# Kernel optimization log

Hardware: AMD Instinct MI355X
Metric: run time of the kernel (lower is better)

The kernel has to match this reference:

```python
import jax, jax.numpy as jnp
import numpy as np

D_MODEL = 1024
MAX_LEN = 2048
BATCH = 4


def _causal_mask(max_len):
    # tril ones -> 0 on/below diag, -inf above (added to scores BEFORE scaling,
    # matching the original module's order of operations)
    return jnp.where(jnp.tril(jnp.ones((max_len, max_len), dtype=bool)), 0.0, -jnp.inf).astype(jnp.float32)


def setup_inputs() -> dict:
    key = jax.random.key(0)
    ks = jax.random.split(key, 9)
    s = 1.0 / np.sqrt(D_MODEL)  # torch Linear default init scale (uniform bound)
    return {
        "encoded_q": jax.random.normal(ks[0], (BATCH, MAX_LEN, D_MODEL), jnp.float32),
        "encoded_k": jax.random.normal(ks[1], (BATCH, MAX_LEN, D_MODEL), jnp.float32),
        "encoded_v": jax.random.normal(ks[2], (BATCH, MAX_LEN, D_MODEL), jnp.float32),
        "W_q": jax.random.uniform(ks[3], (D_MODEL, D_MODEL), jnp.float32, -s, s),
        "b_q": jax.random.uniform(ks[4], (D_MODEL,), jnp.float32, -s, s),
        "W_k": jax.random.uniform(ks[5], (D_MODEL, D_MODEL), jnp.float32, -s, s),
        "b_k": jax.random.uniform(ks[6], (D_MODEL,), jnp.float32, -s, s),
        "W_v": jax.random.uniform(ks[7], (D_MODEL, D_MODEL), jnp.float32, -s, s),
        "b_v": jax.random.uniform(ks[8], (D_MODEL,), jnp.float32, -s, s),
        "parameter_mask": 1,
    }


def reference(encoded_q, encoded_k, encoded_v, W_q, b_q, W_k, b_k, W_v, b_v, parameter_mask):
    # torch Linear: y = x @ W.T + b
    q = jnp.einsum("bsd,ed->bse", encoded_q, W_q) + b_q  # [B,S,D]
    k = jnp.einsum("bsd,ed->bse", encoded_k, W_k) + b_k
    v = jnp.einsum("bsd,ed->bse", encoded_v, W_v) + b_v
    values = jnp.einsum("bqd,bkd->bqk", q, k)  # [B,S,S]
    if parameter_mask:
        values = values + _causal_mask(values.shape[-1])
    scaled = values / jnp.sqrt(jnp.float32(D_MODEL))
    attn = jax.nn.softmax(scaled, axis=-1)
    return jnp.einsum("bqk,bkd->bqd", attn, v)  # [B,S,D]
```

## Files before the change

kernel.cpp:

```cpp
#include <hip/hip_runtime.h>

typedef __bf16 bf16;
typedef __attribute__((ext_vector_type(8))) __bf16 bf16x8;
typedef __attribute__((ext_vector_type(4))) __bf16 bf16x4;
typedef __attribute__((ext_vector_type(4))) float f32x4;

#define S_LEN 2048
#define DM 1024
#define NB 4

__device__ __forceinline__ void async_copy16(const void* g, void* l)
{
    __builtin_amdgcn_global_load_lds(
        (const __attribute__((address_space(1))) unsigned int*)g,
        (__attribute__((address_space(3))) unsigned int*)l,
        16, 0, 0);
}

__device__ __forceinline__ void gemm_tile(
    const bf16* __restrict__ A, int lda,
    const bf16* __restrict__ B, int ldb,
    int kSteps, char* smem, f32x4 (&acc)[4][4])
{
    bf16* sA = (bf16*)smem;
    bf16* sB = (bf16*)(smem + 16384);
    const int tid = threadIdx.x;
    const int w = tid >> 6, lane = tid & 63;
    const int quad = lane >> 4, l16 = lane & 15;
    const int wr = w >> 1, wc = w & 1;

#pragma unroll
    for (int i = 0; i < 4; i++)
#pragma unroll
        for (int j = 0; j < 4; j++) acc[i][j] = f32x4{0.f, 0.f, 0.f, 0.f};

    const int srow = tid >> 3;
    const int sc8  = tid & 7;
    const int srcCol = (sc8 ^ (srow & 7)) * 16;
    const char* aG = (const char*)(A + (size_t)srow * lda) + srcCol;
    const char* bG = (const char*)(B + (size_t)srow * ldb) + srcCol;
    char* aL = (char*)sA + w * 1024;
    char* bL = (char*)sB + w * 1024;
    const size_t aRow32 = (size_t)lda * 64;
    const size_t bRow32 = (size_t)ldb * 64;

    const int swz = l16 & 7;

    for (int ks = 0; ks < kSteps; ks++) {
        const char* aGk = aG + (size_t)ks * 128;
        const char* bGk = bG + (size_t)ks * 128;
#pragma unroll
        for (int i = 0; i < 4; i++) {
            async_copy16(aGk + i * aRow32, aL + i * 4096);
            async_copy16(bGk + i * bRow32, bL + i * 4096);
        }
        __syncthreads();
#pragma unroll
        for (int kk = 0; kk < 2; kk++) {
            bf16x8 af[4], bfr[4];
#pragma unroll
            for (int t = 0; t < 4; t++) {
                const int ca = ((kk * 4 + quad) ^ swz) * 16;
                af[t]  = *(const bf16x8*)((const char*)sA + (wr * 64 + t * 16 + l16) * 128 + ca);
                bfr[t] = *(const bf16x8*)((const char*)sB + (wc * 64 + t * 16 + l16) * 128 + ca);
            }
#pragma unroll
            for (int rt = 0; rt < 4; rt++)
#pragma unroll
                for (int ct = 0; ct < 4; ct++)
                    acc[rt][ct] = __builtin_amdgcn_mfma_f32_16x16x32_bf16(
                        af[rt], bfr[ct], acc[rt][ct], 0, 0, 0);
        }
        __syncthreads();
    }
}

__global__ __launch_bounds__(256) void cvt3_kernel(
    const float* __restrict__ s0, const float* __restrict__ s1, const float* __restrict__ s2,
    bf16* __restrict__ d0, bf16* __restrict__ d1, bf16* __restrict__ d2)
{
    const float* src = blockIdx.y == 0 ? s0 : blockIdx.y == 1 ? s1 : s2;
    bf16* dst        = blockIdx.y == 0 ? d0 : blockIdx.y == 1 ? d1 : d2;
    size_t i = ((size_t)blockIdx.x * 256 + threadIdx.x) * 8;
    f32x4 a = *(const f32x4*)(src + i);
    f32x4 b = *(const f32x4*)(src + i + 4);
    bf16x8 o;
    o[0] = (bf16)a[0]; o[1] = (bf16)a[1]; o[2] = (bf16)a[2]; o[3] = (bf16)a[3];
    o[4] = (bf16)b[0]; o[5] = (bf16)b[1]; o[6] = (bf16)b[2]; o[7] = (bf16)b[3];
    *(bf16x8*)(dst + i) = o;
}

__global__ __launch_bounds__(256) void proj_kernel(
    const bf16* __restrict__ Eq, const bf16* __restrict__ Ek, const bf16* __restrict__ Ev,
    const bf16* __restrict__ Wq, const bf16* __restrict__ Wk, const bf16* __restrict__ Wv,
    const float* __restrict__ bq, const float* __restrict__ bk, const float* __restrict__ bv,
    bf16* __restrict__ Qo, bf16* __restrict__ Ko, bf16* __restrict__ Vt)
{
    __shared__ __align__(16) char smem[34816];
    const int bid = blockIdx.x;
    const int c = bid & 7;
    const int j = bid >> 3;
    const int z = j >> 6;
    const int r64 = j & 63;
    const int mTile = c * 8 + (r64 >> 3);
    const int nTile = r64 & 7;
    const int m0 = mTile * 128, n0 = nTile * 128;

    const bf16* E     = z == 0 ? Eq : z == 1 ? Ek : Ev;
    const bf16* W     = z == 0 ? Wq : z == 1 ? Wk : Wv;
    const float* bias = z == 0 ? bq : z == 1 ? bk : bv;

    f32x4 acc[4][4];
    gemm_tile(E + (size_t)m0 * DM, DM, W + (size_t)n0 * DM, DM, DM / 64, smem, acc);

    const int tid = threadIdx.x;
    const int w = tid >> 6, lane = tid & 63;
    const int quad = lane >> 4, l16 = lane & 15;
    const int wr = w >> 1, wc = w & 1;
    const int nBase = n0 + wc * 64;

    float bcol[4];
#pragma unroll
    for (int ct = 0; ct < 4; ct++) bcol[ct] = bias[nBase + ct * 16 + l16];

    if (z < 2) {
        bf16* Tt = (bf16*)smem;
#pragma unroll
        for (int rt = 0; rt < 4; rt++)
#pragma unroll
            for (int ct = 0; ct < 4; ct++)
#pragma unroll
                for (int r = 0; r < 4; r++)
                    Tt[(wr * 64 + rt * 16 + quad * 4 + r) * 136 + wc * 64 + ct * 16 + l16]
                        = (bf16)(acc[rt][ct][r] + bcol[ct]);
        __syncthreads();
        bf16* O = z == 0 ? Qo : Ko;
        const int row = tid >> 1, half = tid & 1;
        const bf16* src = Tt + row * 136 + half * 64;
        bf16* dst = O + (size_t)(m0 + row) * DM + n0 + half * 64;
#pragma unroll
        for (int i = 0; i < 8; i++)
            *(bf16x8*)(dst + i * 8) = *(const bf16x8*)(src + i * 8);
    } else {
        const int mBase = m0 + wr * 64;
#pragma unroll
        for (int rt = 0; rt < 4; rt++) {
            const int m = mBase + rt * 16 + quad * 4;
            const int bb = m >> 11;
            const int s  = m & 2047;
#pragma unroll
            for (int ct = 0; ct < 4; ct++) {
                const int n = nBase + ct * 16 + l16;
                bf16x4 o;
                o[0] = (bf16)(acc[rt][ct][0] + bcol[ct]);
                o[1] = (bf16)(acc[rt][ct][1] + bcol[ct]);
                o[2] = (bf16)(acc[rt][ct][2] + bcol[ct]);
                o[3] = (bf16)(acc[rt][ct][3] + bcol[ct]);
                *(bf16x4*)(Vt + ((size_t)(bb * DM + n)) * S_LEN + s) = o;
            }
        }
    }
}

__global__ __launch_bounds__(256) void qk_kernel(
    const bf16* __restrict__ Q, const bf16* __restrict__ K,
    const int* __restrict__ maskp, bf16* __restrict__ P, float* __restrict__ lsum)
{
    const int bid = blockIdx.x;
    const int c = bid & 7;
    const int j = bid >> 3;
    const int b = j >> 5;
    const int jj = j & 31;
    const int kt = (jj < 16) ? c : (15 - c);
    const int qt = jj & 15;
    const bool causal = (maskp[0] != 0);
    if (causal && kt > qt) return;

    __shared__ __align__(16) char smem[34816];

    f32x4 acc[4][4];
    const bf16* Qb = Q + ((size_t)(b * S_LEN + qt * 128)) * DM;
    const bf16* Kb = K + ((size_t)(b * S_LEN + kt * 128)) * DM;
    gemm_tile(Qb, DM, Kb, DM, DM / 64, smem, acc);

    const int tid = threadIdx.x;
    const int w = tid >> 6, lane = tid & 63;
    const int quad = lane >> 4, l16 = lane & 15;
    const int wr = w >> 1, wc = w & 1;
    const float scale = 0.03125f;

    bf16* Pt = (bf16*)smem;
#pragma unroll
    for (int rt = 0; rt < 4; rt++)
#pragma unroll
        for (int r = 0; r < 4; r++) {
            const int rloc = wr * 64 + rt * 16 + quad * 4 + r;
            const int qg = qt * 128 + rloc;
#pragma unroll
            for (int ct = 0; ct < 4; ct++) {
                const int kg = kt * 128 + wc * 64 + ct * 16 + l16;
                float p = (!causal || kg <= qg) ? __expf(acc[rt][ct][r] * scale) : 0.0f;
                Pt[rloc * 136 + wc * 64 + ct * 16 + l16] = (bf16)p;
            }
        }
    __syncthreads();

    bf16* Pb = P + (size_t)b * S_LEN * S_LEN;
    float* lb = lsum + b * S_LEN;
    const int row = tid >> 1, half = tid & 1;
    const bf16* src = Pt + row * 136 + half * 64;
    bf16* dst = Pb + (size_t)(qt * 128 + row) * S_LEN + kt * 128 + half * 64;
    float rs = 0.0f;
#pragma unroll
    for (int i = 0; i < 8; i++) {
        bf16x8 x = *(const bf16x8*)(src + i * 8);
        *(bf16x8*)(dst + i * 8) = x;
#pragma unroll
        for (int e = 0; e < 8; e++) rs += (float)x[e];
    }
    rs += __shfl_xor(rs, 1);
    if (half == 0) atomicAdd(&lb[qt * 128 + row], rs);
}

__global__ __launch_bounds__(256) void pv_kernel(
    const bf16* __restrict__ P, const bf16* __restrict__ Vt,
    const float* __restrict__ lsum, const int* __restrict__ maskp,
    float* __restrict__ Out)
{
    const int bid = blockIdx.x;
    const int dt = bid & 7;
    const int j = bid >> 3;
    const int b = j >> 4;
    const int qt = 15 - (j & 15);
    const bool causal = (maskp[0] != 0);
    const int kSteps = causal ? (qt + 1) * 2 : (S_LEN / 64);

    __shared__ __align__(16) char smem[33792];

    f32x4 acc[4][4];
    const bf16* Pb = P + ((size_t)b * S_LEN + qt * 128) * S_LEN;
    const bf16* Vb = Vt + ((size_t)(b * DM + dt * 128)) * S_LEN;
    gemm_tile(Pb, S_LEN, Vb, S_LEN, kSteps, smem, acc);

    const int tid = threadIdx.x;
    const int w = tid >> 6, lane = tid & 63;
    const int quad = lane >> 4, l16 = lane & 15;
    const int wr = w >> 1, wc = w & 1;

    const float* lb = lsum + b * S_LEN;
    float inv[4][4];
#pragma unroll
    for (int rt = 0; rt < 4; rt++)
#pragma unroll
        for (int r = 0; r < 4; r++)
            inv[rt][r] = 1.0f / lb[qt * 128 + wr * 64 + rt * 16 + quad * 4 + r];

    float* Ot = (float*)smem;
#pragma unroll
    for (int h = 0; h < 2; h++) {
        if (wr == h) {
#pragma unroll
            for (int rt = 0; rt < 4; rt++)
#pragma unroll
                for (int r = 0; r < 4; r++) {
                    const int rloc = rt * 16 + quad * 4 + r;
#pragma unroll
                    for (int ct = 0; ct < 4; ct++)
                        Ot[rloc * 132 + wc * 64 + ct * 16 + l16] = acc[rt][ct][r] * inv[rt][r];
                }
        }
        __syncthreads();
        const int row = tid >> 2, qq = tid & 3;
        const float* src = Ot + row * 132 + qq * 32;
        float* dst = Out + (size_t)(b * S_LEN + qt * 128 + h * 64 + row) * DM + dt * 128 + qq * 32;
#pragma unroll
        for (int i = 0; i < 8; i++)
            *(f32x4*)(dst + i * 4) = *(const f32x4*)(src + i * 4);
        __syncthreads();
    }
}

extern "C" void kernel_launch(void* const* d_in, const int* in_sizes, int n_in,
                              void* d_out, int out_size, void* d_ws, size_t ws_size,
                              hipStream_t stream)
{
    const float* Eq = (const float*)d_in[0];
    const float* Ek = (const float*)d_in[1];
    const float* Ev = (const float*)d_in[2];
    const float* Wq = (const float*)d_in[3];
    const float* bq = (const float*)d_in[4];
    const float* Wk = (const float*)d_in[5];
    const float* bk = (const float*)d_in[6];
    const float* Wv = (const float*)d_in[7];
    const float* bv = (const float*)d_in[8];
    const int* maskp = (const int*)d_in[9];
    float* Out = (float*)d_out;

    char* ws = (char*)d_ws;
    const size_t SZ_QKV = (size_t)NB * S_LEN * DM * 2;
    const size_t SZ_W   = (size_t)DM * DM * 2;
    bf16* Qb  = (bf16*)(ws);
    bf16* Kb  = (bf16*)(ws + SZ_QKV);
    bf16* Vtb = (bf16*)(ws + 2 * SZ_QKV);
    bf16* Wqb = (bf16*)(ws + 3 * SZ_QKV);
    bf16* Wkb = (bf16*)(ws + 3 * SZ_QKV + SZ_W);
    bf16* Wvb = (bf16*)(ws + 3 * SZ_QKV + 2 * SZ_W);
    float* lsum = (float*)(ws + 3 * SZ_QKV + 3 * SZ_W);
    bf16* Pbuf = (bf16*)(ws + 3 * SZ_QKV + 3 * SZ_W + (1 << 20));
    bf16* Eqb = Pbuf;
    bf16* Ekb = Eqb + (size_t)NB * S_LEN * DM;
    bf16* Evb = Ekb + (size_t)NB * S_LEN * DM;

    hipMemsetAsync(lsum, 0, (size_t)NB * S_LEN * 4, stream);
    cvt3_kernel<<<dim3(512, 3), 256, 0, stream>>>(Wq, Wk, Wv, Wqb, Wkb, Wvb);
    cvt3_kernel<<<dim3(4096, 3), 256, 0, stream>>>(Eq, Ek, Ev, Eqb, Ekb, Evb);

    proj_kernel<<<1536, 256, 0, stream>>>(
        Eqb, Ekb, Evb, Wqb, Wkb, Wvb, bq, bk, bv, Qb, Kb, Vtb);

    qk_kernel<<<1024, 256, 0, stream>>>(Qb, Kb, maskp, Pbuf, lsum);
    pv_kernel<<<512, 256, 0, stream>>>(Pbuf, Vtb, lsum, maskp, Out);
}
```

Before: 314.3 us.

## Double-buffer LDS tiles in gemm_tile with async prefetch of next k-step

Rewrites the shared GEMM mainloop so each block keeps two LDS buffers. It issues the global-to-LDS async loads for step k+2 while the MFMAs for the current step run, using explicit vmcnt/lgkmcnt waits and raw barriers. The aim is to hide global load latency that the old load-sync-compute-sync loop exposed. In exchange LDS per block grows to 64 KB, which may lower occupancy, and the loop assumes an even kSteps. Extra syncthreads are added before the epilogues reuse shared memory.

```diff
diff --git a/kernel.cpp b/kernel.cpp
--- a/kernel.cpp
+++ b/kernel.cpp
@@ -17,13 +17,58 @@
         16, 0, 0);
 }
 
+#define VM_WAIT8 asm volatile("s_waitcnt vmcnt(8)" ::: "memory")
+#define VM_WAIT0 asm volatile("s_waitcnt vmcnt(0)" ::: "memory")
+#define LGKM0    asm volatile("s_waitcnt lgkmcnt(0)" ::: "memory")
+#define BAR      asm volatile("s_barrier" ::: "memory")
+
+
+__device__ __forceinline__ void stage_issue(const char* aGk, size_t aRow32,
+                                            const char* bGk, size_t bRow32,
+                                            char* aL, char* bL)
+{
+#pragma unroll
+    for (int i = 0; i < 4; i++) {
+        async_copy16(aGk + i * aRow32, aL + i * 4096);
+        async_copy16(bGk + i * bRow32, bL + i * 4096);
+    }
+}
+
+__device__ __forceinline__ void read_frags(const char* bufA, const char* bufB,
+                                           int wr, int wc, int l16, int quad,
+                                           bf16x8 (&af)[2][4], bf16x8 (&bfr)[2][4])
+{
+    const int swz = l16 & 7;
+#pragma unroll
+    for (int kk = 0; kk < 2; kk++) {
+        const int col = (((kk << 2) + quad) ^ swz) << 4;
+#pragma unroll
+        for (int t = 0; t < 4; t++) {
+            af[kk][t]  = *(const bf16x8*)(bufA + (wr * 64 + t * 16 + l16) * 128 + col);
+            bfr[kk][t] = *(const bf16x8*)(bufB + (wc * 64 + t * 16 + l16) * 128 + col);
+        }
+    }
+}
+
+__device__ __forceinline__ void mfma_all(const bf16x8 (&af)[2][4],
+                                         const bf16x8 (&bfr)[2][4],
+                                         f32x4 (&acc)[4][4])
+{
+#pragma unroll
+    for (int kk = 0; kk < 2; kk++)
+#pragma unroll
+        for (int rt = 0; rt < 4; rt++)
+#pragma unroll
+            for (int ct = 0; ct < 4; ct++)
+                acc[rt][ct] = __builtin_amdgcn_mfma_f32_16x16x32_bf16(
+                    af[kk][rt], bfr[kk][ct], acc[rt][ct], 0, 0, 0);
+}
+
 __device__ __forceinline__ void gemm_tile(
     const bf16* __restrict__ A, int lda,
     const bf16* __restrict__ B, int ldb,
     int kSteps, char* smem, f32x4 (&acc)[4][4])
 {
-    bf16* sA = (bf16*)smem;
-    bf16* sB = (bf16*)(smem + 16384);
     const int tid = threadIdx.x;
     const int w = tid >> 6, lane = tid & 63;
     const int quad = lane >> 4, l16 = lane & 15;
@@ -39,39 +84,39 @@
     const int srcCol = (sc8 ^ (srow & 7)) * 16;
     const char* aG = (const char*)(A + (size_t)srow * lda) + srcCol;
     const char* bG = (const char*)(B + (size_t)srow * ldb) + srcCol;
-    char* aL = (char*)sA + w * 1024;
-    char* bL = (char*)sB + w * 1024;
     const size_t aRow32 = (size_t)lda * 64;
     const size_t bRow32 = (size_t)ldb * 64;
-
-    const int swz = l16 & 7;
-
-    for (int ks = 0; ks < kSteps; ks++) {
-        const char* aGk = aG + (size_t)ks * 128;
-        const char* bGk = bG + (size_t)ks * 128;
-#pragma unroll
-        for (int i = 0; i < 4; i++) {
-            async_copy16(aGk + i * aRow32, aL + i * 4096);
-            async_copy16(bGk + i * bRow32, bL + i * 4096);
-        }
-        __syncthreads();
-#pragma unroll
-        for (int kk = 0; kk < 2; kk++) {
-            bf16x8 af[4], bfr[4];
-#pragma unroll
-            for (int t = 0; t < 4; t++) {
-                const int ca = ((kk * 4 + quad) ^ swz) * 16;
-                af[t]  = *(const bf16x8*)((const char*)sA + (wr * 64 + t * 16 + l16) * 128 + ca);
-                bfr[t] = *(const bf16x8*)((const char*)sB + (wc * 64 + t * 16 + l16) * 128 + ca);
-            }
-#pragma unroll
-            for (int rt = 0; rt < 4; rt++)
-#pragma unroll
-                for (int ct = 0; ct < 4; ct++)
-                    acc[rt][ct] = __builtin_amdgcn_mfma_f32_16x16x32_bf16(
-                        af[rt], bfr[ct], acc[rt][ct], 0, 0, 0);
-        }
-        __syncthreads();
+    char* aL0 = smem +     0 + w * 1024;
+    char* bL0 = smem + 16384 + w * 1024;
+    char* aL1 = smem + 32768 + w * 1024;
+    char* bL1 = smem + 49152 + w * 1024;
+
+    stage_issue(aG,       aRow32, bG,       bRow32, aL0, bL0);
+    stage_issue(aG + 128, aRow32, bG + 128, bRow32, aL1, bL1);
+
+    for (int ks = 0; ks < kSteps; ks += 2) {
+        const bool more = (ks + 2 < kSteps);
+        bf16x8 af[2][4], bfr[2][4];
+
+        VM_WAIT8;
+        BAR;
+        read_frags(smem, smem + 16384, wr, wc, l16, quad, af, bfr);
+        LGKM0;
+        BAR;
+        if (more)
+            stage_issue(aG + (size_t)(ks + 2) * 128, aRow32,
+                        bG + (size_t)(ks + 2) * 128, bRow32, aL0, bL0);
+        mfma_all(af, bfr, acc);
+
+        if (more) { VM_WAIT8; } else { VM_WAIT0; }
+        BAR;
+        read_frags(smem + 32768, smem + 49152, wr, wc, l16, quad, af, bfr);
+        LGKM0;
+        BAR;
+        if (more)
+            stage_issue(aG + (size_t)(ks + 3) * 128, aRow32,
+                        bG + (size_t)(ks + 3) * 128, bRow32, aL1, bL1);
+        mfma_all(af, bfr, acc);
     }
 }
 
@@ -96,15 +141,14 @@
     const float* __restrict__ bq, const float* __restrict__ bk, const float* __restrict__ bv,
     bf16* __restrict__ Qo, bf16* __restrict__ Ko, bf16* __restrict__ Vt)
 {
-    __shared__ __align__(16) char smem[34816];
+    __shared__ __align__(16) char smem[65536];
     const int bid = blockIdx.x;
     const int c = bid & 7;
     const int j = bid >> 3;
     const int z = j >> 6;
     const int r64 = j & 63;
-    const int mTile = c * 8 + (r64 >> 3);
-    const int nTile = r64 & 7;
-    const int m0 = mTile * 128, n0 = nTile * 128;
+    const int m0 = (c * 8 + (r64 >> 3)) * 128;
+    const int n0 = (r64 & 7) * 128;
 
     const bf16* E     = z == 0 ? Eq : z == 1 ? Ek : Ev;
     const bf16* W     = z == 0 ? Wq : z == 1 ? Wk : Wv;
@@ -123,6 +167,7 @@
 #pragma unroll
     for (int ct = 0; ct < 4; ct++) bcol[ct] = bias[nBase + ct * 16 + l16];
 
+    __syncthreads();
     if (z < 2) {
         bf16* Tt = (bf16*)smem;
 #pragma unroll
@@ -176,7 +221,7 @@
     const bool causal = (maskp[0] != 0);
     if (causal && kt > qt) return;
 
-    __shared__ __align__(16) char smem[34816];
+    __shared__ __align__(16) char smem[65536];
 
     f32x4 acc[4][4];
     const bf16* Qb = Q + ((size_t)(b * S_LEN + qt * 128)) * DM;
@@ -189,6 +234,7 @@
     const int wr = w >> 1, wc = w & 1;
     const float scale = 0.03125f;
 
+    __syncthreads();
     bf16* Pt = (bf16*)smem;
 #pragma unroll
     for (int rt = 0; rt < 4; rt++)
@@ -235,7 +281,7 @@
     const bool causal = (maskp[0] != 0);
     const int kSteps = causal ? (qt + 1) * 2 : (S_LEN / 64);
 
-    __shared__ __align__(16) char smem[33792];
+    __shared__ __align__(16) char smem[65536];
 
     f32x4 acc[4][4];
     const bf16* Pb = P + ((size_t)b * S_LEN + qt * 128) * S_LEN;
@@ -255,6 +301,7 @@
         for (int r = 0; r < 4; r++)
             inv[rt][r] = 1.0f / lb[qt * 128 + wr * 64 + rt * 16 + quad * 4 + r];
 
+    __syncthreads();
     float* Ot = (float*)smem;
 #pragma unroll
     for (int h = 0; h < 2; h++) {
```

Result: faster. 289.3 us (-7.9%).

## Prefetch next K-tile into registers instead of direct global-to-LDS loads

Applied to the files above, without the earlier changes.

Replaces the global_load_lds async copies in the shared GEMM tile loop with register-staged prefetching. Each step writes the already-loaded registers to LDS, issues the next tile's global loads, and then runs the MFMAs, so global latency overlaps compute. Barriers become raw s_barrier calls, and a __syncthreads is added before each epilogue reuses shared memory. Launch bounds now request 3 waves per SIMD, which limits register use and may cause spills given the extra prefetch registers.

```diff
diff --git a/kernel.cpp b/kernel.cpp
--- a/kernel.cpp
+++ b/kernel.cpp
@@ -4,17 +4,25 @@
 typedef __attribute__((ext_vector_type(8))) __bf16 bf16x8;
 typedef __attribute__((ext_vector_type(4))) __bf16 bf16x4;
 typedef __attribute__((ext_vector_type(4))) float f32x4;
+typedef __attribute__((ext_vector_type(4))) int i32x4;
 
 #define S_LEN 2048
 #define DM 1024
 #define NB 4
 
-__device__ __forceinline__ void async_copy16(const void* g, void* l)
-{
-    __builtin_amdgcn_global_load_lds(
-        (const __attribute__((address_space(1))) unsigned int*)g,
-        (__attribute__((address_space(3))) unsigned int*)l,
-        16, 0, 0);
+#define LGKM0 asm volatile("s_waitcnt lgkmcnt(0)" ::: "memory")
+#define BAR   asm volatile("s_barrier" ::: "memory")
+
+
+__device__ __forceinline__ void mfma16(const bf16x8 (&af)[4], const bf16x8 (&bfr)[4],
+                                       f32x4 (&acc)[4][4])
+{
+#pragma unroll
+    for (int rt = 0; rt < 4; rt++)
+#pragma unroll
+        for (int ct = 0; ct < 4; ct++)
+            acc[rt][ct] = __builtin_amdgcn_mfma_f32_16x16x32_bf16(
+                af[rt], bfr[ct], acc[rt][ct], 0, 0, 0);
 }
 
 __device__ __forceinline__ void gemm_tile(
@@ -22,8 +30,8 @@
     const bf16* __restrict__ B, int ldb,
     int kSteps, char* smem, f32x4 (&acc)[4][4])
 {
-    bf16* sA = (bf16*)smem;
-    bf16* sB = (bf16*)(smem + 16384);
+    char* sA = smem;
+    char* sB = smem + 16384;
     const int tid = threadIdx.x;
     const int w = tid >> 6, lane = tid & 63;
     const int quad = lane >> 4, l16 = lane & 15;
@@ -39,39 +47,46 @@
     const int srcCol = (sc8 ^ (srow & 7)) * 16;
     const char* aG = (const char*)(A + (size_t)srow * lda) + srcCol;
     const char* bG = (const char*)(B + (size_t)srow * ldb) + srcCol;
-    char* aL = (char*)sA + w * 1024;
-    char* bL = (char*)sB + w * 1024;
     const size_t aRow32 = (size_t)lda * 64;
     const size_t bRow32 = (size_t)ldb * 64;
-
     const int swz = l16 & 7;
 
+    i32x4 rA[4], rB[4];
+#pragma unroll
+    for (int i = 0; i < 4; i++) {
+        rA[i] = *(const i32x4*)(aG + i * aRow32);
+        rB[i] = *(const i32x4*)(bG + i * bRow32);
+    }
+
     for (int ks = 0; ks < kSteps; ks++) {
-        const char* aGk = aG + (size_t)ks * 128;
-        const char* bGk = bG + (size_t)ks * 128;
+        if (ks) BAR;
 #pragma unroll
         for (int i = 0; i < 4; i++) {
-            async_copy16(aGk + i * aRow32, aL + i * 4096);
-            async_copy16(bGk + i * bRow32, bL + i * 4096);
-        }
-        __syncthreads();
+            *(i32x4*)(sA + i * 4096 + tid * 16) = rA[i];
+            *(i32x4*)(sB + i * 4096 + tid * 16) = rB[i];
+        }
+        LGKM0;
+        BAR;
+        if (ks + 1 < kSteps) {
+            const char* aGk = aG + (size_t)(ks + 1) * 128;
+            const char* bGk = bG + (size_t)(ks + 1) * 128;
+#pragma unroll
+            for (int i = 0; i < 4; i++) {
+                rA[i] = *(const i32x4*)(aGk + i * aRow32);
+                rB[i] = *(const i32x4*)(bGk + i * bRow32);
+            }
+        }
 #pragma unroll
         for (int kk = 0; kk < 2; kk++) {
+            const int col = (((kk << 2) + quad) ^ swz) << 4;
             bf16x8 af[4], bfr[4];
 #pragma unroll
             for (int t = 0; t < 4; t++) {
-                const int ca = ((kk * 4 + quad) ^ swz) * 16;
-                af[t]  = *(const bf16x8*)((const char*)sA + (wr * 64 + t * 16 + l16) * 128 + ca);
-                bfr[t] = *(const bf16x8*)((const char*)sB + (wc * 64 + t * 16 + l16) * 128 + ca);
+                af[t]  = *(const bf16x8*)(sA + (wr * 64 + t * 16 + l16) * 128 + col);
+                bfr[t] = *(const bf16x8*)(sB + (wc * 64 + t * 16 + l16) * 128 + col);
             }
-#pragma unroll
-            for (int rt = 0; rt < 4; rt++)
-#pragma unroll
-                for (int ct = 0; ct < 4; ct++)
-                    acc[rt][ct] = __builtin_amdgcn_mfma_f32_16x16x32_bf16(
-                        af[rt], bfr[ct], acc[rt][ct], 0, 0, 0);
-        }
-        __syncthreads();
+            mfma16(af, bfr, acc);
+        }
     }
 }
 
@@ -90,7 +105,7 @@
     *(bf16x8*)(dst + i) = o;
 }
 
-__global__ __launch_bounds__(256) void proj_kernel(
+__global__ __launch_bounds__(256, 3) void proj_kernel(
     const bf16* __restrict__ Eq, const bf16* __restrict__ Ek, const bf16* __restrict__ Ev,
     const bf16* __restrict__ Wq, const bf16* __restrict__ Wk, const bf16* __restrict__ Wv,
     const float* __restrict__ bq, const float* __restrict__ bk, const float* __restrict__ bv,
@@ -102,9 +117,8 @@
     const int j = bid >> 3;
     const int z = j >> 6;
     const int r64 = j & 63;
-    const int mTile = c * 8 + (r64 >> 3);
-    const int nTile = r64 & 7;
-    const int m0 = mTile * 128, n0 = nTile * 128;
+    const int m0 = (c * 8 + (r64 >> 3)) * 128;
+    const int n0 = (r64 & 7) * 128;
 
     const bf16* E     = z == 0 ? Eq : z == 1 ? Ek : Ev;
     const bf16* W     = z == 0 ? Wq : z == 1 ? Wk : Wv;
@@ -123,6 +137,7 @@
 #pragma unroll
     for (int ct = 0; ct < 4; ct++) bcol[ct] = bias[nBase + ct * 16 + l16];
 
+    __syncthreads();
     if (z < 2) {
         bf16* Tt = (bf16*)smem;
 #pragma unroll
@@ -162,7 +177,7 @@
     }
 }
 
-__global__ __launch_bounds__(256) void qk_kernel(
+__global__ __launch_bounds__(256, 3) void qk_kernel(
     const bf16* __restrict__ Q, const bf16* __restrict__ K,
     const int* __restrict__ maskp, bf16* __restrict__ P, float* __restrict__ lsum)
 {
@@ -189,6 +204,7 @@
     const int wr = w >> 1, wc = w & 1;
     const float scale = 0.03125f;
 
+    __syncthreads();
     bf16* Pt = (bf16*)smem;
 #pragma unroll
     for (int rt = 0; rt < 4; rt++)
@@ -222,7 +238,7 @@
     if (half == 0) atomicAdd(&lb[qt * 128 + row], rs);
 }
 
-__global__ __launch_bounds__(256) void pv_kernel(
+__global__ __launch_bounds__(256, 3) void pv_kernel(
     const bf16* __restrict__ P, const bf16* __restrict__ Vt,
     const float* __restrict__ lsum, const int* __restrict__ maskp,
     float* __restrict__ Out)
@@ -255,6 +271,7 @@
         for (int r = 0; r < 4; r++)
             inv[rt][r] = 1.0f / lb[qt * 128 + wr * 64 + rt * 16 + quad * 4 + r];
 
+    __syncthreads();
     float* Ot = (float*)smem;
 #pragma unroll
     for (int h = 0; h < 2; h++) {
```

After: 299.3 us. 1.05x faster.
